# Optimization experiments

Measured on AMD Instinct MI355X. Metric: run time of the kernel, lower is better.

The kernel has to match this reference:

```python
import jax, jax.numpy as jnp
import numpy as np

AX = (-2, -1)
LAMBDA = 0.05
ITERS = 6

# torch fft_2d_img  = fftshift(ifft2(ifftshift(x)))  (used in the FORWARD model)
# torch ifft_2d_img = ifftshift(fft2(fftshift(x)))   (used in the ADJOINT model)

def _fwd_xform(x):
    return jnp.fft.fftshift(jnp.fft.ifft2(jnp.fft.ifftshift(x, axes=AX), axes=AX, norm='ortho'), axes=AX)

def _adj_xform(x):
    return jnp.fft.ifftshift(jnp.fft.fft2(jnp.fft.fftshift(x, axes=AX), axes=AX, norm='ortho'), axes=AX)

def _forward_model(img, S, mask):
    # img [b,t,h,w] -> masked multicoil k-space [b,t,c,h,w]
    return mask * _fwd_xform(S * img[:, :, None])

def _adjoint_model(k, S):
    # k [b,t,c,h,w] -> coil-combined image [b,t,h,w]
    return jnp.sum(jnp.conj(S) * _adj_xform(k), axis=2)

def _system_matrix_R(p, S, L, mask):
    # p [b,sv,h,w]; L [b,t,sv]
    expanded = jnp.einsum('bts,bshw->bthw', L, p)
    combined = _adjoint_model(_forward_model(expanded, S, mask), S)
    out = jnp.einsum('bts,bthw->bshw', jnp.conj(L), combined)
    return out + LAMBDA * p

def _cg_solve(b_vec, S, L, mask):
    z0 = jnp.zeros_like(b_vec)
    rs0 = jnp.vdot(b_vec, b_vec)

    def step(carry, _):
        z, r, p, rs_old, done = carry
        Ap = _system_matrix_R(p, S, L, mask)
        alpha = rs_old / (jnp.vdot(p, Ap) + 1e-20)
        z_n = z + alpha * p
        r_n = r - alpha * Ap
        rs_new = jnp.vdot(r_n, r_n)
        p_n = r_n + (rs_new / (rs_old + 1e-20)) * p
        # replicate torch early-break: freeze state once residual is tiny
        z_o = jnp.where(done, z, z_n)
        r_o = jnp.where(done, r, r_n)
        p_o = jnp.where(done, p, p_n)
        rs_o = jnp.where(done, rs_old, rs_new)
        done_n = done | (jnp.abs(rs_o) < 1e-10)
        return (z_o, r_o, p_o, rs_o, done_n), None

    carry0 = (z0, b_vec, b_vec, rs0, jnp.array(False))
    (z, _, _, _, _), _ = jax.lax.scan(step, carry0, None, length=ITERS)
    return z

def setup_inputs() -> dict:
    key = jax.random.key(0)
    ks = jax.random.split(key, 9)
    b, t, c, h, w, sv = 2, 12, 10, 256, 256, 3
    f32 = jnp.float32
    inp = {
        'k_real': jax.random.normal(ks[0], (b, t, c, h, w), f32),
        'k_imag': jax.random.normal(ks[1], (b, t, c, h, w), f32),
        'mo_real': jax.random.normal(ks[2], (b, sv, h, w), f32),
        'mo_imag': jax.random.normal(ks[3], (b, sv, h, w), f32),
        's_real': jax.random.normal(ks[4], (b, 1, c, h, w), f32),
        's_imag': jax.random.normal(ks[5], (b, 1, c, h, w), f32),
        'tb_real': jax.random.normal(ks[6], (b, t, sv), f32),
        'tb_imag': jax.random.normal(ks[7], (b, t, sv), f32),
        'mask': (jax.random.uniform(ks[8], (b, t, 1, h, w)) < 0.35).astype(f32),
    }
    return inp

def reference(k_real, k_imag, mo_real, mo_imag, s_real, s_imag, tb_real, tb_imag, mask):
    Y = k_real + 1j * k_imag          # [b,t,c,h,w]
    MO = mo_real + 1j * mo_imag       # [b,sv,h,w]
    S = s_real + 1j * s_imag          # [b,1,c,h,w]
    L = tb_real + 1j * tb_imag        # [b,t,sv]
    # b = L^H A^H Y + lambda * model_output
    b_vec = jnp.einsum('bts,bthw->bshw', jnp.conj(L), _adjoint_model(Y, S)) + LAMBDA * MO
    z = _cg_solve(b_vec, S, L, mask)  # [b,sv,h,w] complex
    return jnp.stack([z.real, z.imag], axis=-1)  # [b,sv,h,w,2] float32
```

## Files before the change

### kernel.cpp

```cpp
#include <hip/hip_runtime.h>
#include <math.h>

#define HW 65536
#define LAM 0.05f

struct Scal {
  double pap_re, pap_im, rq_re, rq_im, qq;
  double rs_old, al_re, al_im, beta;
  int done, apply, cnt, pad;
};

__device__ __forceinline__ float2 cadd(float2 a, float2 b){ return make_float2(a.x+b.x, a.y+b.y); }
__device__ __forceinline__ float2 csub(float2 a, float2 b){ return make_float2(a.x-b.x, a.y-b.y); }
__device__ __forceinline__ float2 cmul(float2 a, float2 b){
  return make_float2(a.x*b.x - a.y*b.y, a.x*b.y + a.y*b.x);
}
__device__ __forceinline__ float2 cmulj(float2 a, float2 b){
  return make_float2(a.x*b.x + a.y*b.y, a.x*b.y - a.y*b.x);
}
__device__ __forceinline__ int swz(int p){ return p ^ (p>>4); }

__device__ __forceinline__ void wave_lds_sync(){
  __builtin_amdgcn_wave_barrier();
  __asm__ __volatile__("s_waitcnt lgkmcnt(0)" ::: "memory");
  __builtin_amdgcn_wave_barrier();
}

template<int S>
__device__ __forceinline__ void bfly4(float2 x0, float2 x1, float2 x2, float2 x3,
                                      float2& y0, float2& y1, float2& y2, float2& y3){
  float2 a  = cadd(x0,x2), bm = csub(x0,x2);
  float2 c  = cadd(x1,x3), d  = csub(x1,x3);
  float2 jd = make_float2(-(float)S*d.y, (float)S*d.x);
  y0 = cadd(a,c); y2 = csub(a,c); y1 = cadd(bm,jd); y3 = csub(bm,jd);
}

template<int S>
__device__ __forceinline__ void dft16(float2* a){
  const float s_ = (float)S;
  const float2 W1 = make_float2( 0.92387953251f,  s_*0.38268343236f);
  const float2 W2 = make_float2( 0.70710678119f,  s_*0.70710678119f);
  const float2 W3 = make_float2( 0.38268343236f,  s_*0.92387953251f);
  const float2 W4_ = make_float2(0.f,              s_*1.f);
  const float2 W6 = make_float2(-0.70710678119f,  s_*0.70710678119f);
  const float2 W9 = make_float2(-0.92387953251f, -s_*0.38268343236f);
  float2 t[16];
#pragma unroll
  for (int n0=0;n0<4;n0++){
    float2 y0,y1,y2,y3;
    bfly4<S>(a[n0], a[n0+4], a[n0+8], a[n0+12], y0,y1,y2,y3);
    if (n0==1){ y1=cmul(y1,W1); y2=cmul(y2,W2); y3=cmul(y3,W3); }
    if (n0==2){ y1=cmul(y1,W2); y2=cmul(y2,W4_); y3=cmul(y3,W6); }
    if (n0==3){ y1=cmul(y1,W3); y2=cmul(y2,W6); y3=cmul(y3,W9); }
    t[n0*4+0]=y0; t[n0*4+1]=y1; t[n0*4+2]=y2; t[n0*4+3]=y3;
  }
#pragma unroll
  for (int k1=0;k1<4;k1++){
    float2 y0,y1,y2,y3;
    bfly4<S>(t[0*4+k1], t[1*4+k1], t[2*4+k1], t[3*4+k1], y0,y1,y2,y3);
    a[k1+0]=y0; a[k1+4]=y1; a[k1+8]=y2; a[k1+12]=y3;
  }
}

template<int S>
__device__ void fft256_r16(float2* buf, int l){
  float2 a[16];
#pragma unroll
  for (int j=0;j<16;j++) a[j] = buf[swz(l + 16*j)];
  dft16<S>(a);
  float ang = (float)S * 6.2831853071795865f * (float)l * (1.f/256.f);
  float sn, cs; __sincosf(ang, &sn, &cs);
  float2 wstep = make_float2(cs, sn);
  float2 w = wstep;
#pragma unroll
  for (int k=1;k<16;k++){ a[k] = cmul(a[k], w); w = cmul(w, wstep); }
#pragma unroll
  for (int k=0;k<16;k++) buf[swz(16*k + l)] = a[k];
  wave_lds_sync();
#pragma unroll
  for (int j=0;j<16;j++) a[j] = buf[swz(16*l + j)];
  dft16<S>(a);
  wave_lds_sync();
#pragma unroll
  for (int k=0;k<16;k++) buf[swz(l + 16*k)] = a[k];
  wave_lds_sync();
}

__global__ __launch_bounds__(256) void k_w(const float* __restrict__ mask,
                                           const float* __restrict__ tbr,
                                           const float* __restrict__ tbi,
                                           float* __restrict__ Wf,
                                           Scal* sc){
  if (blockIdx.x==0 && blockIdx.y==0 && threadIdx.x==0){
    sc->pap_re=0.0; sc->pap_im=0.0; sc->rq_re=0.0; sc->rq_im=0.0; sc->qq=0.0;
    sc->rs_old=0.0; sc->al_re=0.0; sc->al_im=0.0; sc->beta=0.0;
    sc->done=0; sc->apply=0; sc->cnt=0;
  }
  __shared__ float wtf[9][16][17];
  int tid = threadIdx.x;
  int bx = blockIdx.x;
  int b  = blockIdx.y;
  int u0 = (bx>>4)<<4, v0 = (bx&15)<<4;
  int u_l = tid>>4, v_l = tid&15;
  int pix = (u0+u_l)*256 + (v0+v_l);
  float d0=0,d1=0,d2=0, o01r=0,o01i=0, o02r=0,o02i=0, o12r=0,o12i=0;
#pragma unroll
  for (int t=0;t<12;t++){
    float m = mask[(size_t)(b*12+t)*HW + pix];
    int lb = (b*12+t)*3;
    float l0r = tbr[lb+0], l0i = tbi[lb+0];
    float l1r = tbr[lb+1], l1i = tbi[lb+1];
    float l2r = tbr[lb+2], l2i = tbi[lb+2];
    d0 += m*(l0r*l0r + l0i*l0i);
    d1 += m*(l1r*l1r + l1i*l1i);
    d2 += m*(l2r*l2r + l2i*l2i);
    o01r += m*(l0r*l1r + l0i*l1i); o01i += m*(l0r*l1i - l0i*l1r);
    o02r += m*(l0r*l2r + l0i*l2i); o02i += m*(l0r*l2i - l0i*l2r);
    o12r += m*(l1r*l2r + l1i*l2i); o12i += m*(l1r*l2i - l1i*l2r);
  }
  const float s = 1.0f/65536.0f;
  wtf[0][u_l][v_l] = d0*s;   wtf[1][u_l][v_l] = d1*s;   wtf[2][u_l][v_l] = d2*s;
  wtf[3][u_l][v_l] = o01r*s; wtf[4][u_l][v_l] = o01i*s;
  wtf[5][u_l][v_l] = o02r*s; wtf[6][u_l][v_l] = o02i*s;
  wtf[7][u_l][v_l] = o12r*s; wtf[8][u_l][v_l] = o12i*s;
  __syncthreads();
  int u_l2 = tid&15, v_l2 = tid>>4;
  float* W0 = Wf + (size_t)b*9*HW;
  float4* WA = (float4*)W0;
  float4* WB = (float4*)(W0 + (size_t)4*HW);
  float*  WC = W0 + (size_t)8*HW;
  size_t wb = (size_t)(v0+v_l2)*256 + (u0+u_l2);
  WA[wb] = make_float4(wtf[0][u_l2][v_l2], wtf[1][u_l2][v_l2],
                       wtf[2][u_l2][v_l2], wtf[3][u_l2][v_l2]);
  WB[wb] = make_float4(wtf[4][u_l2][v_l2], wtf[5][u_l2][v_l2],
                       wtf[6][u_l2][v_l2], wtf[7][u_l2][v_l2]);
  WC[wb] = wtf[8][u_l2][v_l2];
}

__global__ __launch_bounds__(640) void k_yrow(const float* __restrict__ kr,
                                              const float* __restrict__ ki,
                                              const float* __restrict__ tbr,
                                              const float* __restrict__ tbi,
                                              float2* __restrict__ bufA){
  __shared__ float2 lb[30*257];
  int tid = threadIdx.x;
  int r = blockIdx.x, b = blockIdx.y;
  {
    int c = tid>>6, px4 = tid&63;
    float ar[3][4], ai[3][4];
#pragma unroll
    for (int s=0;s<3;s++)
#pragma unroll
      for (int j=0;j<4;j++){ ar[s][j]=0.f; ai[s][j]=0.f; }
#pragma unroll
    for (int t=0;t<12;t++){
      size_t off = ((size_t)((b*12+t)*10+c))*HW + (size_t)r*256 + 4*px4;
      float4 yr4 = *(const float4*)(kr + off);
      float4 yi4 = *(const float4*)(ki + off);
      int lbi = (b*12+t)*3;
      float l0r = tbr[lbi+0], l0i = tbi[lbi+0];
      float l1r = tbr[lbi+1], l1i = tbi[lbi+1];
      float l2r = tbr[lbi+2], l2i = tbi[lbi+2];
      float yrj[4] = {yr4.x, yr4.y, yr4.z, yr4.w};
      float yij[4] = {yi4.x, yi4.y, yi4.z, yi4.w};
#pragma unroll
      for (int j=0;j<4;j++){
        float yr = yrj[j], yi = yij[j];
        ar[0][j] += l0r*yr + l0i*yi;  ai[0][j] += l0r*yi - l0i*yr;
        ar[1][j] += l1r*yr + l1i*yi;  ai[1][j] += l1r*yi - l1i*yr;
        ar[2][j] += l2r*yr + l2i*yi;  ai[2][j] += l2r*yi - l2i*yr;
      }
    }
#pragma unroll
    for (int j=0;j<4;j++){
      int px = 4*px4 + j;
      float sg = (((r ^ px) & 1) ? -1.f : 1.f) * (1.f/256.f);
      int sk = swz(px);
#pragma unroll
      for (int s=0;s<3;s++)
        lb[(c*3+s)*257 + sk] = make_float2(ar[s][j]*sg, ai[s][j]*sg);
    }
  }
  __syncthreads();
  int wv = tid>>6, lane = tid&63, g = lane>>4, l = lane&15;
  int tau = 4*wv + g;
  if (tau < 30){
    float2* lw = &lb[tau*257];
    fft256_r16<-1>(lw, l);
    float2* dst = bufA + (size_t)(b*30+tau)*HW + (size_t)r*256;
#pragma unroll
    for (int j=0;j<8;j++){
      int e = 2*(16*j + l);
      float2 e0 = lw[swz(e)], e1 = lw[swz(e+1)];
      *(float4*)(dst + e) = make_float4(e0.x,e0.y,e1.x,e1.y);
    }
  }
}

template<int MODE>
__global__ __launch_bounds__(384) void k_colpass(float2* __restrict__ bufA,
                                                 const float* __restrict__ Wf){
  __shared__ float2 lb[24*257];
  int tid = threadIdx.x;
  int wv = tid>>6, lane = tid&63, g = lane>>4, l = lane&15;
  int j0 = blockIdx.x*8;
  int c = blockIdx.y, b = blockIdx.z;
#pragma unroll
  for (int it=0; it<8; it++){
    int idx = it*384 + tid;
    int s = idx>>10, rem = idx&1023, u = rem>>2, cp = rem&3;
    const float2* src = bufA + (size_t)(b*30 + c*3 + s)*HW;
    float4 v = *(const float4*)(src + u*256 + j0 + 2*cp);
    lb[(s*8+2*cp  )*257 + swz(u)] = make_float2(v.x, v.y);
    lb[(s*8+2*cp+1)*257 + swz(u)] = make_float2(v.z, v.w);
  }
  __syncthreads();
  int tau = 4*wv + g;
  if (MODE==0){
    fft256_r16<-1>(&lb[tau*257], l);
  } else {
    fft256_r16<1>(&lb[tau*257], l);
    __syncthreads();
    const float* W0 = Wf + (size_t)b*9*HW;
    const float4* WA = (const float4*)W0;
    const float4* WB = (const float4*)(W0 + (size_t)4*HW);
    const float*  WC = W0 + (size_t)8*HW;
    for (int idx=tid; idx<2048; idx+=384){
      int u = idx&255, col = idx>>8;
      int su = swz(u);
      int v = j0 + col;
      float2 x0 = lb[(0*8+col)*257 + su];
      float2 x1 = lb[(1*8+col)*257 + su];
      float2 x2 = lb[(2*8+col)*257 + su];
      size_t wb = (size_t)v*256 + u;
      float4 wa = WA[wb];
      float4 wbv = WB[wb];
      float d0 = wa.x, d1 = wa.y, d2 = wa.z, o01r = wa.w;
      float o01i = wbv.x, o02r = wbv.y, o02i = wbv.z, o12r = wbv.w;
      float o12i = WC[wb];
      float2 y0, y1, y2;
      y0.x = d0*x0.x + o01r*x1.x - o01i*x1.y + o02r*x2.x - o02i*x2.y;
      y0.y = d0*x0.y + o01r*x1.y + o01i*x1.x + o02r*x2.y + o02i*x2.x;
      y1.x = o01r*x0.x + o01i*x0.y + d1*x1.x + o12r*x2.x - o12i*x2.y;
      y1.y = o01r*x0.y - o01i*x0.x + d1*x1.y + o12r*x2.y + o12i*x2.x;
      y2.x = o02r*x0.x + o02i*x0.y + o12r*x1.x + o12i*x1.y + d2*x2.x;
      y2.y = o02r*x0.y - o02i*x0.x + o12r*x1.y - o12i*x1.x + d2*x2.y;
      lb[(0*8+col)*257 + su] = y0;
      lb[(1*8+col)*257 + su] = y1;
      lb[(2*8+col)*257 + su] = y2;
    }
    __syncthreads();
    fft256_r16<-1>(&lb[tau*257], l);
  }
  __syncthreads();
#pragma unroll
  for (int it=0; it<8; it++){
    int idx = it*384 + tid;
    int s = idx>>10, rem = idx&1023, u = rem>>2, cp = rem&3;
    float2* dst = bufA + (size_t)(b*30 + c*3 + s)*HW;
    float2 e0 = lb[(s*8+2*cp  )*257 + swz(u)];
    float2 e1 = lb[(s*8+2*cp+1)*257 + swz(u)];
    *(float4*)(dst + u*256 + j0 + 2*cp) = make_float4(e0.x, e0.y, e1.x, e1.y);
  }
}

__global__ __launch_bounds__(256) void k_combine(const float2* __restrict__ bufA,
                                                 const float* __restrict__ sr_,
                                                 const float* __restrict__ si_,
                                                 const float* __restrict__ mor,
                                                 const float* __restrict__ moi,
                                                 float2* __restrict__ z,
                                                 float2* __restrict__ r,
                                                 float2* __restrict__ p,
                                                 Scal* sc){
  __shared__ double sd[4];
  int tid = threadIdx.x;
  int i = blockIdx.x*256 + tid;
  int pix = i & (HW-1);
  int bs = i >> 16;
  int b = bs/3, s = bs - 3*b;
  float2 acc = make_float2(0.f, 0.f);
#pragma unroll
  for (int c=0;c<10;c++){
    float2 F  = bufA[(size_t)(b*30 + c*3 + s)*HW + pix];
    size_t so = (size_t)(b*10+c)*HW + pix;
    float2 sv = make_float2(sr_[so], si_[so]);
    acc = cadd(acc, cmulj(sv, F));
  }
  float sgl = (((pix>>8)^pix)&1 ? -1.f : 1.f) * LAM;
  acc.x += sgl*mor[i]; acc.y += sgl*moi[i];
  z[i] = make_float2(0.f,0.f);
  r[i] = acc; p[i] = acc;
  double dre = (double)acc.x*acc.x + (double)acc.y*acc.y;
  for (int off=32; off>0; off>>=1) dre += __shfl_down(dre, off, 64);
  if ((tid&63)==0) sd[tid>>6] = dre;
  __syncthreads();
  if (tid==0) atomicAdd(&sc->rs_old, sd[0]+sd[1]+sd[2]+sd[3]);
}

__global__ __launch_bounds__(512) void k_spfft(float2* __restrict__ p,
                                               float2* __restrict__ rvec,
                                               float2* __restrict__ z,
                                               const float2* __restrict__ Ap,
                                               const float* __restrict__ sr_,
                                               const float* __restrict__ si_,
                                               float2* __restrict__ bufA,
                                               Scal* sc){
  __shared__ float2 lb[30*257];
  __shared__ float2 pbuf[3][256];
  int tid = threadIdx.x;
  int wv = tid>>6, lane = tid&63, g = lane>>4, l = lane&15;
  int r = blockIdx.x, b = blockIdx.y;
  int ap = sc->apply;
  float2 alpha = make_float2((float)sc->al_re, (float)sc->al_im);
  float beta = (float)sc->beta;
  for (int i = tid; i < 768; i += 512){
    int s = i>>8, px = i&255;
    size_t oi = (size_t)(b*3+s)*HW + (size_t)r*256 + px;
    float2 pvv = p[oi];
    if (ap){
      float2 zv = z[oi], rv = rvec[oi], apv = Ap[oi];
      zv = cadd(zv, cmul(alpha, pvv));
      rv = csub(rv, cmul(alpha, apv));
      float2 pn = make_float2(rv.x + beta*pvv.x, rv.y + beta*pvv.y);
      z[oi] = zv; rvec[oi] = rv; p[oi] = pn;
      pvv = pn;
    }
    pbuf[s][px] = pvv;
  }
  __syncthreads();
  {
    int px = tid & 255, h = tid >> 8, sk = swz(px);
    float2 pv0 = pbuf[0][px], pv1 = pbuf[1][px], pv2 = pbuf[2][px];
#pragma unroll
    for (int k=0;k<5;k++){
      int c = h + 2*k;
      size_t so = (size_t)(b*10+c)*HW + (size_t)r*256 + px;
      float2 sv = make_float2(sr_[so], si_[so]);
      lb[(c*3+0)*257 + sk] = cmul(sv, pv0);
      lb[(c*3+1)*257 + sk] = cmul(sv, pv1);
      lb[(c*3+2)*257 + sk] = cmul(sv, pv2);
    }
  }
  __syncthreads();
  int tau = 4*wv + g;
  if (tau < 30){
    float2* lw = &lb[tau*257];
    fft256_r16<1>(lw, l);
    float2* dst = bufA + (size_t)(b*30+tau)*HW + (size_t)r*256;
#pragma unroll
    for (int j=0;j<8;j++){
      int e = 2*(16*j + l);
      float2 e0 = lw[swz(e)], e1 = lw[swz(e+1)];
      *(float4*)(dst + e) = make_float4(e0.x,e0.y,e1.x,e1.y);
    }
  }
}

__global__ __launch_bounds__(512) void k_rowcomb(const float2* __restrict__ bufA,
                                                 const float* __restrict__ sr_,
                                                 const float* __restrict__ si_,
                                                 const float2* __restrict__ pvec,
                                                 const float2* __restrict__ rvec,
                                                 float2* __restrict__ Ap,
                                                 Scal* sc){
  __shared__ float2 lb[30*257];
  __shared__ float2 part[3][256];
  __shared__ double sd[5][4];
  int tid = threadIdx.x;
  int wv = tid>>6, lane = tid&63, g = lane>>4, l = lane&15;
  int r = blockIdx.x, b = blockIdx.y;
  int tau = 4*wv + g;
  if (tau < 30){
    const float2* src = bufA + (size_t)(b*30+tau)*HW + (size_t)r*256;
    float2* lw = &lb[tau*257];
#pragma unroll
    for (int j=0;j<8;j++){
      int e = 2*(16*j + l);
      float4 v = *(const float4*)(src + e);
      lw[swz(e)]   = make_float2(v.x, v.y);
      lw[swz(e+1)] = make_float2(v.z, v.w);
    }
    wave_lds_sync();
    fft256_r16<-1>(lw, l);
  }
  __syncthreads();
  int px = tid & 255, h = tid >> 8, sk = swz(px);
  float2 a0={0,0}, a1={0,0}, a2={0,0};
#pragma unroll
  for (int k=0;k<5;k++){
    int c = h + 2*k;
    size_t so = (size_t)(b*10+c)*HW + (size_t)r*256 + px;
    float2 sv = make_float2(sr_[so], si_[so]);
    a0 = cadd(a0, cmulj(sv, lb[(c*3+0)*257 + sk]));
    a1 = cadd(a1, cmulj(sv, lb[(c*3+1)*257 + sk]));
    a2 = cadd(a2, cmulj(sv, lb[(c*3+2)*257 + sk]));
  }
  if (h==1){ part[0][px]=a0; part[1][px]=a1; part[2][px]=a2; }
  __syncthreads();
  double d0=0.0, d1=0.0, d2=0.0, d3=0.0, d4=0.0;
  if (tid < 256){
    a0 = cadd(a0, part[0][px]);
    a1 = cadd(a1, part[1][px]);
    a2 = cadd(a2, part[2][px]);
    float2 accs[3] = {a0,a1,a2};
#pragma unroll
    for (int s=0;s<3;s++){
      size_t oi = (size_t)(b*3+s)*HW + (size_t)r*256 + px;
      float2 acc = accs[s];
      float2 av = pvec[oi];
      float2 rv = rvec[oi];
      acc.x += LAM*av.x; acc.y += LAM*av.y;
      Ap[oi] = acc;
      d0 += (double)av.x*acc.x + (double)av.y*acc.y;
      d1 += (double)av.x*acc.y - (double)av.y*acc.x;
      d2 += (double)rv.x*acc.x + (double)rv.y*acc.y;
      d3 += (double)rv.x*acc.y - (double)rv.y*acc.x;
      d4 += (double)acc.x*acc.x + (double)acc.y*acc.y;
    }
  }
  for (int off=32; off>0; off>>=1){
    d0 += __shfl_down(d0, off, 64);
    d1 += __shfl_down(d1, off, 64);
    d2 += __shfl_down(d2, off, 64);
    d3 += __shfl_down(d3, off, 64);
    d4 += __shfl_down(d4, off, 64);
  }
  if (lane==0 && wv<4){ sd[0][wv]=d0; sd[1][wv]=d1; sd[2][wv]=d2; sd[3][wv]=d3; sd[4][wv]=d4; }
  __syncthreads();
  if (tid==0){
    double t0=0,t1=0,t2=0,t3=0,t4=0;
#pragma unroll
    for (int q=0;q<4;q++){ t0+=sd[0][q]; t1+=sd[1][q]; t2+=sd[2][q]; t3+=sd[3][q]; t4+=sd[4][q]; }
    atomicAdd(&sc->pap_re, t0); atomicAdd(&sc->pap_im, t1);
    atomicAdd(&sc->rq_re,  t2); atomicAdd(&sc->rq_im,  t3);
    atomicAdd(&sc->qq,     t4);
    int total = (int)(gridDim.x*gridDim.y);
    int prev = atomicAdd(&sc->cnt, 1);
    if (prev == total-1){
      sc->cnt = 0;
      if (!sc->done){
        double pr = sc->pap_re + 1e-20, pi = sc->pap_im;
        double den = pr*pr + pi*pi;
        double rs = sc->rs_old;
        double alr =  rs*pr/den, ali = -rs*pi/den;
        double rs_new = rs - 2.0*(alr*sc->rq_re - ali*sc->rq_im)
                           + (alr*alr + ali*ali)*sc->qq;
        sc->al_re = alr; sc->al_im = ali;
        sc->beta = rs_new/(rs + 1e-20);
        sc->rs_old = rs_new;
        sc->apply = 1;
        if (fabs(rs_new) < 1e-10) sc->done = 1;
      } else {
        sc->apply = 0;
      }
      sc->pap_re=0.0; sc->pap_im=0.0; sc->rq_re=0.0; sc->rq_im=0.0; sc->qq=0.0;
    }
  }
}

__global__ __launch_bounds__(256) void k_out(const float2* __restrict__ z,
                                             const float2* __restrict__ p,
                                             const Scal* sc,
                                             float* __restrict__ out){
  int i = blockIdx.x*256 + threadIdx.x;
  int pix = i & (HW-1);
  float sgn = (((pix>>8)^pix)&1) ? -1.f : 1.f;
  float2 zv = z[i];
  if (sc->apply){
    float2 alpha = make_float2((float)sc->al_re, (float)sc->al_im);
    zv = cadd(zv, cmul(alpha, p[i]));
  }
  out[2*i]   = sgn*zv.x;
  out[2*i+1] = sgn*zv.y;
}

extern "C" void kernel_launch(void* const* d_in, const int* in_sizes, int n_in,
                              void* d_out, int out_size, void* d_ws, size_t ws_size,
                              hipStream_t stream){
  const float* kr   = (const float*)d_in[0];
  const float* ki   = (const float*)d_in[1];
  const float* mor  = (const float*)d_in[2];
  const float* moi  = (const float*)d_in[3];
  const float* sr   = (const float*)d_in[4];
  const float* si   = (const float*)d_in[5];
  const float* tbr  = (const float*)d_in[6];
  const float* tbi  = (const float*)d_in[7];
  const float* mask = (const float*)d_in[8];
  float* out = (float*)d_out;

  float2* ws   = (float2*)d_ws;
  float2* bufA = ws;
  float*  Wf   = (float*)(ws + 3932160);
  float2* z    = ws + 4521984;
  float2* r    = ws + 4915200;
  float2* p    = ws + 5308416;
  float2* Ap   = ws + 5701632;
  Scal*   sc   = (Scal*)(ws + 6094848);

  k_w<<<dim3(256,2),dim3(256),0,stream>>>(mask, tbr, tbi, Wf, sc);
  k_yrow<<<dim3(256,2),dim3(640),0,stream>>>(kr, ki, tbr, tbi, bufA);
  k_colpass<0><<<dim3(32,10,2),dim3(384),0,stream>>>(bufA, Wf);
  k_combine<<<dim3(1536),dim3(256),0,stream>>>(bufA, sr, si, mor, moi,
                                               z, r, p, sc);
  for (int it=0; it<6; ++it){
    k_spfft<<<dim3(256,2),dim3(512),0,stream>>>(p, r, z, Ap, sr, si, bufA, sc);
    k_colpass<1><<<dim3(32,10,2),dim3(384),0,stream>>>(bufA, Wf);
    k_rowcomb<<<dim3(256,2),dim3(512),0,stream>>>(bufA, sr, si, p, r, Ap, sc);
  }
  k_out<<<dim3(1536),dim3(256),0,stream>>>(z, p, sc, out);
}
```

Measured before the change: 722.8 us.

## Fuse row-combine with next spread-FFT via grid-wide barrier inside kernel

Merges the row-combine, CG update and next iteration's coil-spread row FFT into one kernel, using an in-kernel grid barrier (atomic counter spin-wait) so every block sees the reduced dot products before updating z/r/p. This removes the Ap buffer round trip and one launch per iteration. Each block recomputes the CG scalar recurrence from per-iteration accumulators instead of relying on a single last-block update. It depends on all 512 blocks being co-resident (launch_bounds 512,4). The spin loop has a guard that could silently break out if blocks are not resident.

```diff
diff --git a/kernel.cpp b/kernel.cpp
--- a/kernel.cpp
+++ b/kernel.cpp
@@ -4,10 +4,10 @@
 #define HW 65536
 #define LAM 0.05f
 
-struct Scal {
-  double pap_re, pap_im, rq_re, rq_im, qq;
-  double rs_old, al_re, al_im, beta;
-  int done, apply, cnt, pad;
+struct ScalN {
+  double rs0;
+  double pap_re[6], pap_im[6], rq_re[6], rq_im[6], qq[6];
+  int cnt; int pad;
 };
 
 __device__ __forceinline__ float2 cadd(float2 a, float2 b){ return make_float2(a.x+b.x, a.y+b.y); }
@@ -90,11 +90,9 @@
                                            const float* __restrict__ tbr,
                                            const float* __restrict__ tbi,
                                            float* __restrict__ Wf,
-                                           Scal* sc){
-  if (blockIdx.x==0 && blockIdx.y==0 && threadIdx.x==0){
-    sc->pap_re=0.0; sc->pap_im=0.0; sc->rq_re=0.0; sc->rq_im=0.0; sc->qq=0.0;
-    sc->rs_old=0.0; sc->al_re=0.0; sc->al_im=0.0; sc->beta=0.0;
-    sc->done=0; sc->apply=0; sc->cnt=0;
+                                           ScalN* sc){
+  if (blockIdx.x==0 && blockIdx.y==0 && threadIdx.x < (int)(sizeof(ScalN)/8)){
+    ((double*)sc)[threadIdx.x] = 0.0;
   }
   __shared__ float wtf[9][16][17];
   int tid = threadIdx.x;
@@ -272,7 +270,7 @@
                                                  float2* __restrict__ z,
                                                  float2* __restrict__ r,
                                                  float2* __restrict__ p,
-                                                 Scal* sc){
+                                                 ScalN* sc){
   __shared__ double sd[4];
   int tid = threadIdx.x;
   int i = blockIdx.x*256 + tid;
@@ -295,38 +293,21 @@
   for (int off=32; off>0; off>>=1) dre += __shfl_down(dre, off, 64);
   if ((tid&63)==0) sd[tid>>6] = dre;
   __syncthreads();
-  if (tid==0) atomicAdd(&sc->rs_old, sd[0]+sd[1]+sd[2]+sd[3]);
-}
-
-__global__ __launch_bounds__(512) void k_spfft(float2* __restrict__ p,
-                                               float2* __restrict__ rvec,
-                                               float2* __restrict__ z,
-                                               const float2* __restrict__ Ap,
-                                               const float* __restrict__ sr_,
-                                               const float* __restrict__ si_,
-                                               float2* __restrict__ bufA,
-                                               Scal* sc){
+  if (tid==0) atomicAdd(&sc->rs0, sd[0]+sd[1]+sd[2]+sd[3]);
+}
+
+__global__ __launch_bounds__(512) void k_sp0(const float2* __restrict__ p,
+                                             const float* __restrict__ sr_,
+                                             const float* __restrict__ si_,
+                                             float2* __restrict__ bufA){
   __shared__ float2 lb[30*257];
   __shared__ float2 pbuf[3][256];
   int tid = threadIdx.x;
   int wv = tid>>6, lane = tid&63, g = lane>>4, l = lane&15;
   int r = blockIdx.x, b = blockIdx.y;
-  int ap = sc->apply;
-  float2 alpha = make_float2((float)sc->al_re, (float)sc->al_im);
-  float beta = (float)sc->beta;
   for (int i = tid; i < 768; i += 512){
     int s = i>>8, px = i&255;
-    size_t oi = (size_t)(b*3+s)*HW + (size_t)r*256 + px;
-    float2 pvv = p[oi];
-    if (ap){
-      float2 zv = z[oi], rv = rvec[oi], apv = Ap[oi];
-      zv = cadd(zv, cmul(alpha, pvv));
-      rv = csub(rv, cmul(alpha, apv));
-      float2 pn = make_float2(rv.x + beta*pvv.x, rv.y + beta*pvv.y);
-      z[oi] = zv; rvec[oi] = rv; p[oi] = pn;
-      pvv = pn;
-    }
-    pbuf[s][px] = pvv;
+    pbuf[s][px] = p[(size_t)(b*3+s)*HW + (size_t)r*256 + px];
   }
   __syncthreads();
   {
@@ -357,16 +338,18 @@
   }
 }
 
-__global__ __launch_bounds__(512) void k_rowcomb(const float2* __restrict__ bufA,
-                                                 const float* __restrict__ sr_,
-                                                 const float* __restrict__ si_,
-                                                 const float2* __restrict__ pvec,
-                                                 const float2* __restrict__ rvec,
-                                                 float2* __restrict__ Ap,
-                                                 Scal* sc){
+__global__ __launch_bounds__(512,4) void k_rowspfft(float2* __restrict__ bufA,
+                                                    const float* __restrict__ sr_,
+                                                    const float* __restrict__ si_,
+                                                    float2* __restrict__ pvec,
+                                                    float2* __restrict__ rvec,
+                                                    float2* __restrict__ zvec,
+                                                    ScalN* sc,
+                                                    int itr, int last){
   __shared__ float2 lb[30*257];
-  __shared__ float2 part[3][256];
+  __shared__ float2 pb[3][256];
   __shared__ double sd[5][4];
+  __shared__ float sca[4];
   int tid = threadIdx.x;
   int wv = tid>>6, lane = tid&63, g = lane>>4, l = lane&15;
   int r = blockIdx.x, b = blockIdx.y;
@@ -396,26 +379,27 @@
     a1 = cadd(a1, cmulj(sv, lb[(c*3+1)*257 + sk]));
     a2 = cadd(a2, cmulj(sv, lb[(c*3+2)*257 + sk]));
   }
-  if (h==1){ part[0][px]=a0; part[1][px]=a1; part[2][px]=a2; }
-  __syncthreads();
+  if (h==1){ pb[0][px]=a0; pb[1][px]=a1; pb[2][px]=a2; }
+  __syncthreads();
+  float2 pv[3], rv[3], ap3[3];
   double d0=0.0, d1=0.0, d2=0.0, d3=0.0, d4=0.0;
   if (tid < 256){
-    a0 = cadd(a0, part[0][px]);
-    a1 = cadd(a1, part[1][px]);
-    a2 = cadd(a2, part[2][px]);
+    a0 = cadd(a0, pb[0][px]);
+    a1 = cadd(a1, pb[1][px]);
+    a2 = cadd(a2, pb[2][px]);
     float2 accs[3] = {a0,a1,a2};
 #pragma unroll
     for (int s=0;s<3;s++){
       size_t oi = (size_t)(b*3+s)*HW + (size_t)r*256 + px;
       float2 acc = accs[s];
       float2 av = pvec[oi];
-      float2 rv = rvec[oi];
+      float2 rvv = rvec[oi];
       acc.x += LAM*av.x; acc.y += LAM*av.y;
-      Ap[oi] = acc;
+      pv[s] = av; rv[s] = rvv; ap3[s] = acc;
       d0 += (double)av.x*acc.x + (double)av.y*acc.y;
       d1 += (double)av.x*acc.y - (double)av.y*acc.x;
-      d2 += (double)rv.x*acc.x + (double)rv.y*acc.y;
-      d3 += (double)rv.x*acc.y - (double)rv.y*acc.x;
+      d2 += (double)rvv.x*acc.x + (double)rvv.y*acc.y;
+      d3 += (double)rvv.x*acc.y - (double)rvv.y*acc.x;
       d4 += (double)acc.x*acc.x + (double)acc.y*acc.y;
     }
   }
@@ -432,45 +416,93 @@
     double t0=0,t1=0,t2=0,t3=0,t4=0;
 #pragma unroll
     for (int q=0;q<4;q++){ t0+=sd[0][q]; t1+=sd[1][q]; t2+=sd[2][q]; t3+=sd[3][q]; t4+=sd[4][q]; }
-    atomicAdd(&sc->pap_re, t0); atomicAdd(&sc->pap_im, t1);
-    atomicAdd(&sc->rq_re,  t2); atomicAdd(&sc->rq_im,  t3);
-    atomicAdd(&sc->qq,     t4);
-    int total = (int)(gridDim.x*gridDim.y);
-    int prev = atomicAdd(&sc->cnt, 1);
-    if (prev == total-1){
-      sc->cnt = 0;
-      if (!sc->done){
-        double pr = sc->pap_re + 1e-20, pi = sc->pap_im;
+    atomicAdd(&sc->pap_re[itr], t0); atomicAdd(&sc->pap_im[itr], t1);
+    atomicAdd(&sc->rq_re[itr],  t2); atomicAdd(&sc->rq_im[itr],  t3);
+    atomicAdd(&sc->qq[itr],     t4);
+    __threadfence();
+    atomicAdd(&sc->cnt, 1);
+    int target = (int)(gridDim.x*gridDim.y) * (itr+1);
+    long guard = 0;
+    while (__hip_atomic_load(&sc->cnt, __ATOMIC_ACQUIRE, __HIP_MEMORY_SCOPE_AGENT) < target){
+      __builtin_amdgcn_s_sleep(2);
+      if (++guard > (1L<<22)) break;
+    }
+    double rs = __hip_atomic_load(&sc->rs0, __ATOMIC_RELAXED, __HIP_MEMORY_SCOPE_AGENT);
+    double alr=0.0, ali=0.0, beta=0.0;
+    int done = 0, applied = 0;
+    for (int j=0; j<=itr; ++j){
+      if (!done){
+        double pr = __hip_atomic_load(&sc->pap_re[j], __ATOMIC_RELAXED, __HIP_MEMORY_SCOPE_AGENT) + 1e-20;
+        double pi = __hip_atomic_load(&sc->pap_im[j], __ATOMIC_RELAXED, __HIP_MEMORY_SCOPE_AGENT);
+        double rqr= __hip_atomic_load(&sc->rq_re[j],  __ATOMIC_RELAXED, __HIP_MEMORY_SCOPE_AGENT);
+        double rqi= __hip_atomic_load(&sc->rq_im[j],  __ATOMIC_RELAXED, __HIP_MEMORY_SCOPE_AGENT);
+        double qq = __hip_atomic_load(&sc->qq[j],     __ATOMIC_RELAXED, __HIP_MEMORY_SCOPE_AGENT);
         double den = pr*pr + pi*pi;
-        double rs = sc->rs_old;
-        double alr =  rs*pr/den, ali = -rs*pi/den;
-        double rs_new = rs - 2.0*(alr*sc->rq_re - ali*sc->rq_im)
-                           + (alr*alr + ali*ali)*sc->qq;
-        sc->al_re = alr; sc->al_im = ali;
-        sc->beta = rs_new/(rs + 1e-20);
-        sc->rs_old = rs_new;
-        sc->apply = 1;
-        if (fabs(rs_new) < 1e-10) sc->done = 1;
+        alr =  rs*pr/den; ali = -rs*pi/den;
+        double rs_new = rs - 2.0*(alr*rqr - ali*rqi) + (alr*alr + ali*ali)*qq;
+        beta = rs_new/(rs + 1e-20);
+        rs = rs_new;
+        applied = 1;
+        if (fabs(rs) < 1e-10) done = 1;
       } else {
-        sc->apply = 0;
+        applied = 0;
       }
-      sc->pap_re=0.0; sc->pap_im=0.0; sc->rq_re=0.0; sc->rq_im=0.0; sc->qq=0.0;
+    }
+    sca[0]=(float)alr; sca[1]=(float)ali; sca[2]=(float)beta; sca[3]=(float)applied;
+  }
+  __syncthreads();
+  float2 alpha = make_float2(sca[0], sca[1]);
+  float beta = sca[2];
+  int applied = sca[3] != 0.f;
+  if (tid < 256 && applied){
+#pragma unroll
+    for (int s=0;s<3;s++){
+      size_t oi = (size_t)(b*3+s)*HW + (size_t)r*256 + px;
+      float2 zv = zvec[oi];
+      zv = cadd(zv, cmul(alpha, pv[s]));
+      zvec[oi] = zv;
+      float2 rn = csub(rv[s], cmul(alpha, ap3[s]));
+      rvec[oi] = rn;
+      float2 pn = make_float2(rn.x + beta*pv[s].x, rn.y + beta*pv[s].y);
+      pvec[oi] = pn;
+      pv[s] = pn;
+    }
+  }
+  if (last) return;
+  if (tid < 256){ pb[0][px]=pv[0]; pb[1][px]=pv[1]; pb[2][px]=pv[2]; }
+  __syncthreads();
+  {
+    float2 pv0 = pb[0][px], pv1 = pb[1][px], pv2 = pb[2][px];
+#pragma unroll
+    for (int k=0;k<5;k++){
+      int c = h + 2*k;
+      size_t so = (size_t)(b*10+c)*HW + (size_t)r*256 + px;
+      float2 sv = make_float2(sr_[so], si_[so]);
+      lb[(c*3+0)*257 + sk] = cmul(sv, pv0);
+      lb[(c*3+1)*257 + sk] = cmul(sv, pv1);
+      lb[(c*3+2)*257 + sk] = cmul(sv, pv2);
+    }
+  }
+  __syncthreads();
+  if (tau < 30){
+    float2* lw = &lb[tau*257];
+    fft256_r16<1>(lw, l);
+    float2* dst = bufA + (size_t)(b*30+tau)*HW + (size_t)r*256;
+#pragma unroll
+    for (int j=0;j<8;j++){
+      int e = 2*(16*j + l);
+      float2 e0 = lw[swz(e)], e1 = lw[swz(e+1)];
+      *(float4*)(dst + e) = make_float4(e0.x,e0.y,e1.x,e1.y);
     }
   }
 }
 
 __global__ __launch_bounds__(256) void k_out(const float2* __restrict__ z,
-                                             const float2* __restrict__ p,
-                                             const Scal* sc,
                                              float* __restrict__ out){
   int i = blockIdx.x*256 + threadIdx.x;
   int pix = i & (HW-1);
   float sgn = (((pix>>8)^pix)&1) ? -1.f : 1.f;
   float2 zv = z[i];
-  if (sc->apply){
-    float2 alpha = make_float2((float)sc->al_re, (float)sc->al_im);
-    zv = cadd(zv, cmul(alpha, p[i]));
-  }
   out[2*i]   = sgn*zv.x;
   out[2*i+1] = sgn*zv.y;
 }
@@ -495,18 +527,18 @@
   float2* z    = ws + 4521984;
   float2* r    = ws + 4915200;
   float2* p    = ws + 5308416;
-  float2* Ap   = ws + 5701632;
-  Scal*   sc   = (Scal*)(ws + 6094848);
+  ScalN*  sc   = (ScalN*)(ws + 6094848);
 
   k_w<<<dim3(256,2),dim3(256),0,stream>>>(mask, tbr, tbi, Wf, sc);
   k_yrow<<<dim3(256,2),dim3(640),0,stream>>>(kr, ki, tbr, tbi, bufA);
   k_colpass<0><<<dim3(32,10,2),dim3(384),0,stream>>>(bufA, Wf);
   k_combine<<<dim3(1536),dim3(256),0,stream>>>(bufA, sr, si, mor, moi,
                                                z, r, p, sc);
+  k_sp0<<<dim3(256,2),dim3(512),0,stream>>>(p, sr, si, bufA);
   for (int it=0; it<6; ++it){
-    k_spfft<<<dim3(256,2),dim3(512),0,stream>>>(p, r, z, Ap, sr, si, bufA, sc);
     k_colpass<1><<<dim3(32,10,2),dim3(384),0,stream>>>(bufA, Wf);
-    k_rowcomb<<<dim3(256,2),dim3(512),0,stream>>>(bufA, sr, si, p, r, Ap, sc);
-  }
-  k_out<<<dim3(1536),dim3(256),0,stream>>>(z, p, sc, out);
-}
+    k_rowspfft<<<dim3(256,2),dim3(512),0,stream>>>(bufA, sr, si, p, r, z,
+                                                   sc, it, it==5 ? 1 : 0);
+  }
+  k_out<<<dim3(1536),dim3(256),0,stream>>>(z, out);
+}
```

After: 917.5 us. 1.27x slower.

## Fuse initial combine with first coil-expand row FFT and hoist coil-map loads

Applied to the files above, without the earlier changes.

Replaces the standalone combine kernel with a row-blocked kernel that coil-combines the adjoint data, forms the initial residual and search direction, and then immediately performs the first coil-expansion row FFT. This removes one launch and a round trip of p through global memory for the first CG iteration. Separately, coil-map, p and r loads in the spfft and rowcomb kernels are issued at kernel start so their latency overlaps the FFT and LDS staging. The cost is higher register pressure from the hoisted values. The fused kernel also depends on row-wise data from the column pass matching the old element-wise indexing, including the shift sign rule.

```diff
diff --git a/kernel.cpp b/kernel.cpp
--- a/kernel.cpp
+++ b/kernel.cpp
@@ -264,38 +264,109 @@
   }
 }
 
-__global__ __launch_bounds__(256) void k_combine(const float2* __restrict__ bufA,
-                                                 const float* __restrict__ sr_,
-                                                 const float* __restrict__ si_,
-                                                 const float* __restrict__ mor,
-                                                 const float* __restrict__ moi,
-                                                 float2* __restrict__ z,
-                                                 float2* __restrict__ r,
-                                                 float2* __restrict__ p,
-                                                 Scal* sc){
-  __shared__ double sd[4];
+__global__ __launch_bounds__(512) void k_bsp(const float* __restrict__ sr_,
+                                             const float* __restrict__ si_,
+                                             const float* __restrict__ mor,
+                                             const float* __restrict__ moi,
+                                             float2* __restrict__ z,
+                                             float2* __restrict__ rvec,
+                                             float2* __restrict__ p,
+                                             float2* __restrict__ bufA,
+                                             Scal* sc){
+  __shared__ float2 lb[30*257];
+  __shared__ float2 pb[3][256];
+  __shared__ double sd[8];
   int tid = threadIdx.x;
-  int i = blockIdx.x*256 + tid;
-  int pix = i & (HW-1);
-  int bs = i >> 16;
-  int b = bs/3, s = bs - 3*b;
-  float2 acc = make_float2(0.f, 0.f);
-#pragma unroll
-  for (int c=0;c<10;c++){
-    float2 F  = bufA[(size_t)(b*30 + c*3 + s)*HW + pix];
-    size_t so = (size_t)(b*10+c)*HW + pix;
-    float2 sv = make_float2(sr_[so], si_[so]);
-    acc = cadd(acc, cmulj(sv, F));
-  }
-  float sgl = (((pix>>8)^pix)&1 ? -1.f : 1.f) * LAM;
-  acc.x += sgl*mor[i]; acc.y += sgl*moi[i];
-  z[i] = make_float2(0.f,0.f);
-  r[i] = acc; p[i] = acc;
-  double dre = (double)acc.x*acc.x + (double)acc.y*acc.y;
+  int wv = tid>>6, lane = tid&63, g = lane>>4, l = lane&15;
+  int r = blockIdx.x, b = blockIdx.y;
+  int px = tid & 255, h = tid >> 8, sk = swz(px);
+  float2 sv5[5];
+#pragma unroll
+  for (int k=0;k<5;k++){
+    int c = h + 2*k;
+    size_t so = (size_t)(b*10+c)*HW + (size_t)r*256 + px;
+    sv5[k] = make_float2(sr_[so], si_[so]);
+  }
+  float mo_r[3], mo_i[3];
+  if (h==0){
+#pragma unroll
+    for (int s=0;s<3;s++){
+      size_t oi = (size_t)(b*3+s)*HW + (size_t)r*256 + px;
+      mo_r[s] = mor[oi]; mo_i[s] = moi[oi];
+    }
+  }
+  int tau = 4*wv + g;
+  if (tau < 30){
+    const float2* src = bufA + (size_t)(b*30+tau)*HW + (size_t)r*256;
+    float2* lw = &lb[tau*257];
+#pragma unroll
+    for (int j=0;j<8;j++){
+      int e = 2*(16*j + l);
+      float4 v = *(const float4*)(src + e);
+      lw[swz(e)]   = make_float2(v.x, v.y);
+      lw[swz(e+1)] = make_float2(v.z, v.w);
+    }
+  }
+  __syncthreads();
+  float2 a0={0,0}, a1={0,0}, a2={0,0};
+#pragma unroll
+  for (int k=0;k<5;k++){
+    a0 = cadd(a0, cmulj(sv5[k], lb[((h+2*k)*3+0)*257 + sk]));
+    a1 = cadd(a1, cmulj(sv5[k], lb[((h+2*k)*3+1)*257 + sk]));
+    a2 = cadd(a2, cmulj(sv5[k], lb[((h+2*k)*3+2)*257 + sk]));
+  }
+  if (h==1){ pb[0][px]=a0; pb[1][px]=a1; pb[2][px]=a2; }
+  __syncthreads();
+  double dre = 0.0;
+  if (h==0){
+    a0 = cadd(a0, pb[0][px]);
+    a1 = cadd(a1, pb[1][px]);
+    a2 = cadd(a2, pb[2][px]);
+    float sgl = (((r ^ px) & 1) ? -1.f : 1.f) * LAM;
+    a0.x += sgl*mo_r[0]; a0.y += sgl*mo_i[0];
+    a1.x += sgl*mo_r[1]; a1.y += sgl*mo_i[1];
+    a2.x += sgl*mo_r[2]; a2.y += sgl*mo_i[2];
+    float2 accs[3] = {a0,a1,a2};
+#pragma unroll
+    for (int s=0;s<3;s++){
+      size_t oi = (size_t)(b*3+s)*HW + (size_t)r*256 + px;
+      z[oi] = make_float2(0.f,0.f);
+      rvec[oi] = accs[s]; p[oi] = accs[s];
+      dre += (double)accs[s].x*accs[s].x + (double)accs[s].y*accs[s].y;
+    }
+    pb[0][px]=a0; pb[1][px]=a1; pb[2][px]=a2;
+  }
   for (int off=32; off>0; off>>=1) dre += __shfl_down(dre, off, 64);
-  if ((tid&63)==0) sd[tid>>6] = dre;
-  __syncthreads();
-  if (tid==0) atomicAdd(&sc->rs_old, sd[0]+sd[1]+sd[2]+sd[3]);
+  if (lane==0) sd[wv] = dre;
+  __syncthreads();
+  if (tid==0){
+    double t=0;
+#pragma unroll
+    for (int q=0;q<8;q++) t += sd[q];
+    atomicAdd(&sc->rs_old, t);
+  }
+  {
+    float2 pv0 = pb[0][px], pv1 = pb[1][px], pv2 = pb[2][px];
+#pragma unroll
+    for (int k=0;k<5;k++){
+      int c = h + 2*k;
+      lb[(c*3+0)*257 + sk] = cmul(sv5[k], pv0);
+      lb[(c*3+1)*257 + sk] = cmul(sv5[k], pv1);
+      lb[(c*3+2)*257 + sk] = cmul(sv5[k], pv2);
+    }
+  }
+  __syncthreads();
+  if (tau < 30){
+    float2* lw = &lb[tau*257];
+    fft256_r16<1>(lw, l);
+    float2* dst = bufA + (size_t)(b*30+tau)*HW + (size_t)r*256;
+#pragma unroll
+    for (int j=0;j<8;j++){
+      int e = 2*(16*j + l);
+      float2 e0 = lw[swz(e)], e1 = lw[swz(e+1)];
+      *(float4*)(dst + e) = make_float4(e0.x,e0.y,e1.x,e1.y);
+    }
+  }
 }
 
 __global__ __launch_bounds__(512) void k_spfft(float2* __restrict__ p,
@@ -311,12 +382,20 @@
   int tid = threadIdx.x;
   int wv = tid>>6, lane = tid&63, g = lane>>4, l = lane&15;
   int r = blockIdx.x, b = blockIdx.y;
+  int px = tid & 255, h = tid >> 8, sk = swz(px);
+  float2 sv5[5];
+#pragma unroll
+  for (int k=0;k<5;k++){
+    int c = h + 2*k;
+    size_t so = (size_t)(b*10+c)*HW + (size_t)r*256 + px;
+    sv5[k] = make_float2(sr_[so], si_[so]);
+  }
   int ap = sc->apply;
   float2 alpha = make_float2((float)sc->al_re, (float)sc->al_im);
   float beta = (float)sc->beta;
   for (int i = tid; i < 768; i += 512){
-    int s = i>>8, px = i&255;
-    size_t oi = (size_t)(b*3+s)*HW + (size_t)r*256 + px;
+    int s = i>>8, ppx = i&255;
+    size_t oi = (size_t)(b*3+s)*HW + (size_t)r*256 + ppx;
     float2 pvv = p[oi];
     if (ap){
       float2 zv = z[oi], rv = rvec[oi], apv = Ap[oi];
@@ -326,20 +405,17 @@
       z[oi] = zv; rvec[oi] = rv; p[oi] = pn;
       pvv = pn;
     }
-    pbuf[s][px] = pvv;
+    pbuf[s][ppx] = pvv;
   }
   __syncthreads();
   {
-    int px = tid & 255, h = tid >> 8, sk = swz(px);
     float2 pv0 = pbuf[0][px], pv1 = pbuf[1][px], pv2 = pbuf[2][px];
 #pragma unroll
     for (int k=0;k<5;k++){
       int c = h + 2*k;
-      size_t so = (size_t)(b*10+c)*HW + (size_t)r*256 + px;
-      float2 sv = make_float2(sr_[so], si_[so]);
-      lb[(c*3+0)*257 + sk] = cmul(sv, pv0);
-      lb[(c*3+1)*257 + sk] = cmul(sv, pv1);
-      lb[(c*3+2)*257 + sk] = cmul(sv, pv2);
+      lb[(c*3+0)*257 + sk] = cmul(sv5[k], pv0);
+      lb[(c*3+1)*257 + sk] = cmul(sv5[k], pv1);
+      lb[(c*3+2)*257 + sk] = cmul(sv5[k], pv2);
     }
   }
   __syncthreads();
@@ -370,6 +446,22 @@
   int tid = threadIdx.x;
   int wv = tid>>6, lane = tid&63, g = lane>>4, l = lane&15;
   int r = blockIdx.x, b = blockIdx.y;
+  int px = tid & 255, h = tid >> 8, sk = swz(px);
+  float2 sv5[5];
+#pragma unroll
+  for (int k=0;k<5;k++){
+    int c = h + 2*k;
+    size_t so = (size_t)(b*10+c)*HW + (size_t)r*256 + px;
+    sv5[k] = make_float2(sr_[so], si_[so]);
+  }
+  float2 av3[3], rv3[3];
+  if (h==0){
+#pragma unroll
+    for (int s=0;s<3;s++){
+      size_t oi = (size_t)(b*3+s)*HW + (size_t)r*256 + px;
+      av3[s] = pvec[oi]; rv3[s] = rvec[oi];
+    }
+  }
   int tau = 4*wv + g;
   if (tau < 30){
     const float2* src = bufA + (size_t)(b*30+tau)*HW + (size_t)r*256;
@@ -385,16 +477,12 @@
     fft256_r16<-1>(lw, l);
   }
   __syncthreads();
-  int px = tid & 255, h = tid >> 8, sk = swz(px);
   float2 a0={0,0}, a1={0,0}, a2={0,0};
 #pragma unroll
   for (int k=0;k<5;k++){
-    int c = h + 2*k;
-    size_t so = (size_t)(b*10+c)*HW + (size_t)r*256 + px;
-    float2 sv = make_float2(sr_[so], si_[so]);
-    a0 = cadd(a0, cmulj(sv, lb[(c*3+0)*257 + sk]));
-    a1 = cadd(a1, cmulj(sv, lb[(c*3+1)*257 + sk]));
-    a2 = cadd(a2, cmulj(sv, lb[(c*3+2)*257 + sk]));
+    a0 = cadd(a0, cmulj(sv5[k], lb[((h+2*k)*3+0)*257 + sk]));
+    a1 = cadd(a1, cmulj(sv5[k], lb[((h+2*k)*3+1)*257 + sk]));
+    a2 = cadd(a2, cmulj(sv5[k], lb[((h+2*k)*3+2)*257 + sk]));
   }
   if (h==1){ part[0][px]=a0; part[1][px]=a1; part[2][px]=a2; }
   __syncthreads();
@@ -408,8 +496,8 @@
     for (int s=0;s<3;s++){
       size_t oi = (size_t)(b*3+s)*HW + (size_t)r*256 + px;
       float2 acc = accs[s];
-      float2 av = pvec[oi];
-      float2 rv = rvec[oi];
+      float2 av = av3[s];
+      float2 rv = rv3[s];
       acc.x += LAM*av.x; acc.y += LAM*av.y;
       Ap[oi] = acc;
       d0 += (double)av.x*acc.x + (double)av.y*acc.y;
@@ -501,10 +589,11 @@
   k_w<<<dim3(256,2),dim3(256),0,stream>>>(mask, tbr, tbi, Wf, sc);
   k_yrow<<<dim3(256,2),dim3(640),0,stream>>>(kr, ki, tbr, tbi, bufA);
   k_colpass<0><<<dim3(32,10,2),dim3(384),0,stream>>>(bufA, Wf);
-  k_combine<<<dim3(1536),dim3(256),0,stream>>>(bufA, sr, si, mor, moi,
-                                               z, r, p, sc);
+  k_bsp<<<dim3(256,2),dim3(512),0,stream>>>(sr, si, mor, moi, z, r, p,
+                                            bufA, sc);
   for (int it=0; it<6; ++it){
-    k_spfft<<<dim3(256,2),dim3(512),0,stream>>>(p, r, z, Ap, sr, si, bufA, sc);
+    if (it > 0)
+      k_spfft<<<dim3(256,2),dim3(512),0,stream>>>(p, r, z, Ap, sr, si, bufA, sc);
     k_colpass<1><<<dim3(32,10,2),dim3(384),0,stream>>>(bufA, Wf);
     k_rowcomb<<<dim3(256,2),dim3(512),0,stream>>>(bufA, sr, si, p, r, Ap, sc);
   }
```

Measured after the change: 719.7 us (median of 2 runs). About the same (-0.4%).
